# Kernel tuning notes

Measured on AMD Instinct MI355X. Metric: run time of the kernel, lower is better.

## Reference

```python
import jax, jax.numpy as jnp
import numpy as np

T = 16          # timesteps
BATCH = 8       # video clips -> leading dim of x is BATCH*T = 128
C_IN = 768      # fixed by nn.Conv2d(768, redu_dim, 1)
D = 256         # redu_dim
K = 64          # num_centers
H = W = 28
EPS = 1e-12     # torch F.normalize eps


def _conv(x, w, padding):
    # x: [N,C,H,W], w: [O,I,kh,kw]
    return jax.lax.conv_general_dilated(
        x, w, window_strides=(1, 1), padding=padding,
        dimension_numbers=('NCHW', 'OIHW', 'NCHW'))


def setup_inputs() -> dict:
    key = jax.random.key(0)
    ks = jax.random.split(key, 9)
    x = jax.random.normal(ks[0], (BATCH * T, C_IN, H, W), dtype=jnp.float32)
    redu_w = jax.random.normal(ks[1], (D, C_IN, 1, 1), jnp.float32) * 0.02
    redu_b = jnp.zeros((D,), jnp.float32)
    share_w = jax.random.normal(ks[2], (K, D, 1, 1), jnp.float32) * 0.05
    share_b = jnp.zeros((K,), jnp.float32)
    U_z = jax.random.normal(ks[3], (K, K, 3, 3), jnp.float32) * 0.04
    U_r = jax.random.normal(ks[4], (K, K, 3, 3), jnp.float32) * 0.04
    U_h = jax.random.normal(ks[5], (K, K, 3, 3), jnp.float32) * 0.04
    centers = jax.random.normal(ks[6], (K, D), jnp.float32) * 0.06
    return {"x": x, "redu_w": redu_w, "redu_b": redu_b,
            "share_w": share_w, "share_b": share_b,
            "U_z": U_z, "U_r": U_r, "U_h": U_h,
            "centers": centers, "timesteps": T}


def reference(x, redu_w, redu_b, share_w, share_b, U_z, U_r, U_h, centers, timesteps):
    t = timesteps
    bt, _, h, w = x.shape
    b = bt // t
    k = share_w.shape[0]
    d = redu_w.shape[0]

    # channel reduction (1x1 conv)
    xr = _conv(x, redu_w, 'VALID') + redu_b[None, :, None, None]        # [bt,d,h,w]
    # shared assignment logits (1x1 conv)
    wxb = _conv(xr, share_w, 'VALID') + share_b[None, :, None, None]     # [bt,k,h,w]
    wxb = wxb.reshape(b, t, k, h, w).transpose(1, 0, 2, 3, 4)            # [t,b,k,h,w]

    # sequential ConvGRU over timesteps
    h0 = jnp.zeros((b, k, h, w), x.dtype)
    def step(h_tm1, w_t):
        z = jax.nn.sigmoid(w_t + _conv(h_tm1, U_z, 'SAME'))
        r = jax.nn.sigmoid(w_t + _conv(h_tm1, U_r, 'SAME'))
        hh = jnp.tanh(w_t + _conv(r * h_tm1, U_h, 'SAME'))
        h_new = (1.0 - z) * hh + z * h_tm1
        return h_new, h_new
    _, hs = jax.lax.scan(step, h0, wxb)                                  # [t,b,k,h,w]

    assign = hs.transpose(1, 0, 2, 3, 4).reshape(b * t, k, h * w)        # [bt,k,hw]
    # softmax over centers per spatial location
    assign = jax.nn.softmax(assign, axis=1)

    # VLAD aggregation
    a_sum = assign.sum(axis=-1, keepdims=True)                           # [bt,k,1]
    a = a_sum * centers[None]                                            # [bt,k,d]
    xf = xr.reshape(b * t, d, h * w)                                     # [bt,d,hw]
    vlad = jnp.einsum('bkp,bdp->bkd', assign, xf) - a                    # [bt,k,d]

    vlad = vlad.reshape(b, t, k, d).sum(axis=1)                          # [b,k,d]
    # intra-norm over feature dim, then global L2 norm
    vlad = vlad / jnp.maximum(jnp.linalg.norm(vlad, axis=2, keepdims=True), EPS)
    vlad = vlad.reshape(b, k * d)
    vlad = vlad / jnp.maximum(jnp.linalg.norm(vlad, axis=1, keepdims=True), EPS)
    return vlad
```

## Files before the change

kernel.cpp:

```cpp
#include <hip/hip_runtime.h>
#include <hip/hip_bf16.h>

#define T_ 16
#define B_ 8
#define CIN 768
#define D_ 256
#define K_ 64
#define HW 784
#define W_ 28

typedef short short8 __attribute__((ext_vector_type(8)));
typedef short short4v __attribute__((ext_vector_type(4)));
typedef float floatx4 __attribute__((ext_vector_type(4)));
typedef unsigned short ushort_t;

__device__ __forceinline__ unsigned short f2bf(float x) {
    union { float f; unsigned u; } v; v.f = x;
    unsigned u = v.u;
    unsigned r = (u + 0x7fffu + ((u >> 16) & 1u)) >> 16;
    return (unsigned short)r;
}
__device__ __forceinline__ float bf2f(unsigned short h) {
    union { unsigned u; float f; } v; v.u = ((unsigned)h) << 16; return v.f;
}

__device__ __forceinline__ float block_reduce_sum_256(float v) {
    for (int off = 32; off > 0; off >>= 1) v += __shfl_down(v, off, 64);
    __shared__ float red[4];
    __shared__ float tot;
    int lane = threadIdx.x & 63, wid = threadIdx.x >> 6;
    if (lane == 0) red[wid] = v;
    __syncthreads();
    if (threadIdx.x == 0) tot = red[0] + red[1] + red[2] + red[3];
    __syncthreads();
    return tot;
}

__global__ __launch_bounds__(256) void cvt_weights(
    const float* __restrict__ rw, const float* __restrict__ sw,
    const float* __restrict__ Uz, const float* __restrict__ Ur,
    const float* __restrict__ Uh,
    ushort_t* __restrict__ whi, ushort_t* __restrict__ wlo,
    ushort_t* __restrict__ shi, ushort_t* __restrict__ slo,
    ushort_t* __restrict__ azh, ushort_t* __restrict__ azl,
    ushort_t* __restrict__ ahh, ushort_t* __restrict__ ahl)
{
    int i = blockIdx.x * 256 + threadIdx.x;
    const int nR = D_ * CIN;
    const int nS = K_ * D_;
    const int nZR = 128 * 576;
    const int nH = 64 * 576;
    if (i < nR) {
        float x = rw[i];
        unsigned short h = f2bf(x);
        whi[i] = h; wlo[i] = f2bf(x - bf2f(h));
    } else if (i < nR + nS) {
        int j = i - nR;
        float x = sw[j];
        unsigned short h = f2bf(x);
        shi[j] = h; slo[j] = f2bf(x - bf2f(h));
    } else if (i < nR + nS + nZR) {
        int j = i - nR - nS;
        int row = j / 576, kk = j - row * 576;
        int tap = kk >> 6, c = kk & 63;
        const float* U = (row < 64) ? Uz : Ur;
        float x = U[(((size_t)(row & 63)) * 64 + c) * 9 + tap];
        unsigned short h = f2bf(x);
        azh[j] = h; azl[j] = f2bf(x - bf2f(h));
    } else if (i < nR + nS + nZR + nH) {
        int j = i - nR - nS - nZR;
        int row = j / 576, kk = j - row * 576;
        int tap = kk >> 6, c = kk & 63;
        float x = Uh[(((size_t)row) * 64 + c) * 9 + tap];
        unsigned short h = f2bf(x);
        ahh[j] = h; ahl[j] = f2bf(x - bf2f(h));
    }
}

template<int MTOT, int BM, int KD, int MINW>
__global__ __launch_bounds__(256, MINW) void mfma_conv1x1(
    const float* __restrict__ X, const ushort_t* __restrict__ Whi,
    const ushort_t* __restrict__ Wlo, const float* __restrict__ bias,
    float* __restrict__ Out)
{
    const int nt = blockIdx.x, mt = blockIdx.y, bt = blockIdx.z;
    const int p0 = nt * 112, m0 = mt * BM;
    const int tid = threadIdx.x, lane = tid & 63, wv = tid >> 6;
    const int li = lane & 15, koff = (lane >> 4) * 8;
    constexpr int MI = BM / 64;
    constexpr int NKS = KD / 32;
    const float* Xb = X + (size_t)bt * KD * HW;
    float* Ob = Out + (size_t)bt * MTOT * HW;

    __shared__ ushort_t lB[2][112 * 40];

    floatx4 acc[MI][7];
#pragma unroll
    for (int a = 0; a < MI; ++a)
#pragma unroll
        for (int b = 0; b < 7; ++b) acc[a][b] = (floatx4){0.f, 0.f, 0.f, 0.f};

    const int mbase = m0 + wv * (MI * 16);

    const int u0j = tid / 112, u0p = tid - u0j * 112;
    const bool u1v = tid < 192;
    const int u1j = (tid + 256) / 112, u1p = (tid + 256) - u1j * 112;

    float b0[16], b1[16];
    short8 ahi[MI], alo[MI];

    auto loadB = [&](int k0, float* bb) {
        const float* xp0 = Xb + (size_t)(k0 + u0j * 8) * HW + p0 + u0p;
#pragma unroll
        for (int c = 0; c < 8; ++c) bb[c] = xp0[(size_t)c * HW];
        if (u1v) {
            const float* xp1 = Xb + (size_t)(k0 + u1j * 8) * HW + p0 + u1p;
#pragma unroll
            for (int c = 0; c < 8; ++c) bb[8 + c] = xp1[(size_t)c * HW];
        }
    };
    auto writeB = [&](const float* bb) {
        short8 vh, vl;
#pragma unroll
        for (int c = 0; c < 8; ++c) {
            unsigned short h = f2bf(bb[c]);
            vh[c] = (short)h; vl[c] = (short)f2bf(bb[c] - bf2f(h));
        }
        *(short8*)&lB[0][u0p * 40 + u0j * 8] = vh;
        *(short8*)&lB[1][u0p * 40 + u0j * 8] = vl;
        if (u1v) {
#pragma unroll
            for (int c = 0; c < 8; ++c) {
                unsigned short h = f2bf(bb[8 + c]);
                vh[c] = (short)h; vl[c] = (short)f2bf(bb[8 + c] - bf2f(h));
            }
            *(short8*)&lB[0][u1p * 40 + u1j * 8] = vh;
            *(short8*)&lB[1][u1p * 40 + u1j * 8] = vl;
        }
    };
    auto loadA = [&](int k0) {
#pragma unroll
        for (int mi = 0; mi < MI; ++mi) {
            int m = mbase + mi * 16 + li;
            ahi[mi] = *(const short8*)(Whi + (size_t)m * KD + k0 + koff);
            alo[mi] = *(const short8*)(Wlo + (size_t)m * KD + k0 + koff);
        }
    };
    auto domfma = [&]() {
#pragma unroll
        for (int ni = 0; ni < 7; ++ni) {
            int n = ni * 16 + li;
            short8 bhi = *(const short8*)&lB[0][n * 40 + koff];
            short8 blo = *(const short8*)&lB[1][n * 40 + koff];
#pragma unroll
            for (int mi = 0; mi < MI; ++mi) {
                acc[mi][ni] = __builtin_amdgcn_mfma_f32_16x16x32_bf16(ahi[mi], bhi, acc[mi][ni], 0, 0, 0);
                acc[mi][ni] = __builtin_amdgcn_mfma_f32_16x16x32_bf16(ahi[mi], blo, acc[mi][ni], 0, 0, 0);
                acc[mi][ni] = __builtin_amdgcn_mfma_f32_16x16x32_bf16(alo[mi], bhi, acc[mi][ni], 0, 0, 0);
            }
        }
    };

    loadB(0, b0);
    for (int ks = 0; ks < NKS; ks += 2) {
        loadA(ks * 32);
        writeB(b0);
        __syncthreads();
        if (ks + 1 < NKS) loadB((ks + 1) * 32, b1);
        domfma();
        __syncthreads();
        loadA((ks + 1) * 32);
        writeB(b1);
        __syncthreads();
        if (ks + 2 < NKS) loadB((ks + 2) * 32, b0);
        domfma();
        __syncthreads();
    }

#pragma unroll
    for (int mi = 0; mi < MI; ++mi) {
        int m0g = mbase + mi * 16 + ((lane >> 4) << 2);
#pragma unroll
        for (int ni = 0; ni < 7; ++ni) {
            int p = p0 + ni * 16 + li;
#pragma unroll
            for (int r = 0; r < 4; ++r)
                Ob[(size_t)(m0g + r) * HW + p] = acc[mi][ni][r] + bias[m0g + r];
        }
    }
}

__global__ __launch_bounds__(512, 2) void gru_step(
    const ushort_t* __restrict__ hRhi, const ushort_t* __restrict__ hRlo,
    ushort_t* __restrict__ hWhi, ushort_t* __restrict__ hWlo,
    const ushort_t* __restrict__ azh, const ushort_t* __restrict__ azl,
    const ushort_t* __restrict__ ahh, const ushort_t* __restrict__ ahl,
    const float* __restrict__ wxb, float* __restrict__ hs_t, int t)
{
    const int y0 = blockIdx.x, b = blockIdx.y;
    const int tid = threadIdx.x, lane = tid & 63, wv = tid >> 6;
    const int li = lane & 15, koff8 = (lane >> 4) * 8, kq = (lane >> 4) * 4;

    __shared__ ushort_t Hhi[5 * 30 * 72], Hlo[5 * 30 * 72];
    __shared__ ushort_t Rhi[3 * 30 * 72], Rlo[3 * 30 * 72];
    __shared__ float zs[28 * 68];

    {
        const ushort_t* gh = hRhi + (size_t)b * HW * 64;
        const ushort_t* gl = hRlo + (size_t)b * HW * 64;
        for (int e = tid; e < 1200; e += 512) {
            int r = e / 240, rem = e - r * 240;
            int lx = rem >> 3, j = rem & 7;
            int gy = y0 - 2 + r, gx = lx - 1;
            short8 vh = {0,0,0,0,0,0,0,0}, vl = {0,0,0,0,0,0,0,0};
            if (gy >= 0 && gy < 28 && gx >= 0 && gx < 28) {
                size_t go = ((size_t)(gy * 28 + gx)) * 64 + j * 8;
                vh = *(const short8*)(gh + go);
                vl = *(const short8*)(gl + go);
            }
            int lo = (r * 30 + lx) * 72 + j * 8;
            *(short8*)&Hhi[lo] = vh;
            *(short8*)&Hlo[lo] = vl;
        }
        short8 z8 = {0,0,0,0,0,0,0,0};
        for (int e = tid; e < 1620; e += 512) {
            if (e < 810) *(short8*)&Rhi[e * 8] = z8;
            else         *(short8*)&Rlo[(e - 810) * 8] = z8;
        }
    }
    __syncthreads();

    const float* wx = wxb + ((size_t)(b * T_ + t) * K_) * HW;
    const int c0 = li;
    const int c1 = (li < 12) ? 16 + li : 0;

    if (wv < 4) {
        const int kb = wv * 16;
        const ushort_t* Ah = azh + (size_t)(kb + li) * 576;
        const ushort_t* Al = azl + (size_t)(kb + li) * 576;
        floatx4 az[2];
        az[0] = (floatx4){0.f,0.f,0.f,0.f}; az[1] = (floatx4){0.f,0.f,0.f,0.f};
#pragma unroll
        for (int tap = 0; tap < 9; ++tap) {
            const int dy = tap / 3, dx = tap - dy * 3;
#pragma unroll
            for (int ch = 0; ch < 2; ++ch) {
                short8 whi_ = *(const short8*)(Ah + tap * 64 + ch * 32 + koff8);
                short8 wlo_ = *(const short8*)(Al + tap * 64 + ch * 32 + koff8);
                int cb = ch * 32 + koff8;
                int o0 = ((dy + 1) * 30 + c0 + dx) * 72 + cb;
                int o1 = ((dy + 1) * 30 + c1 + dx) * 72 + cb;
                short8 bh0 = *(const short8*)&Hhi[o0];
                short8 bl0 = *(const short8*)&Hlo[o0];
                short8 bh1 = *(const short8*)&Hhi[o1];
                short8 bl1 = *(const short8*)&Hlo[o1];
                az[0] = __builtin_amdgcn_mfma_f32_16x16x32_bf16(whi_, bh0, az[0], 0, 0, 0);
                az[0] = __builtin_amdgcn_mfma_f32_16x16x32_bf16(whi_, bl0, az[0], 0, 0, 0);
                az[0] = __builtin_amdgcn_mfma_f32_16x16x32_bf16(wlo_, bh0, az[0], 0, 0, 0);
                az[1] = __builtin_amdgcn_mfma_f32_16x16x32_bf16(whi_, bh1, az[1], 0, 0, 0);
                az[1] = __builtin_amdgcn_mfma_f32_16x16x32_bf16(whi_, bl1, az[1], 0, 0, 0);
                az[1] = __builtin_amdgcn_mfma_f32_16x16x32_bf16(wlo_, bh1, az[1], 0, 0, 0);
            }
        }
        const int kb4 = kb + kq;
#pragma unroll
        for (int cf = 0; cf < 2; ++cf) {
            int c = cf * 16 + li;
            if (c < 28) {
                floatx4 zv;
#pragma unroll
                for (int r = 0; r < 4; ++r)
                    zv[r] = 1.f / (1.f + __expf(-(wx[(size_t)(kb4 + r) * HW + y0 * 28 + c] + az[cf][r])));
                *(floatx4*)&zs[c * 68 + kb4] = zv;
            }
        }
    } else {
        const int kb = (wv - 4) * 16;
        const ushort_t* Ah = azh + (size_t)(64 + kb + li) * 576;
        const ushort_t* Al = azl + (size_t)(64 + kb + li) * 576;
        floatx4 ar[3][2];
#pragma unroll
        for (int i = 0; i < 3; ++i) {
            ar[i][0] = (floatx4){0.f,0.f,0.f,0.f};
            ar[i][1] = (floatx4){0.f,0.f,0.f,0.f};
        }
        __builtin_amdgcn_s_setprio(1);
#pragma unroll
        for (int tap = 0; tap < 9; ++tap) {
            const int dy = tap / 3, dx = tap - dy * 3;
#pragma unroll
            for (int ch = 0; ch < 2; ++ch) {
                short8 whi_ = *(const short8*)(Ah + tap * 64 + ch * 32 + koff8);
                short8 wlo_ = *(const short8*)(Al + tap * 64 + ch * 32 + koff8);
                int cb = ch * 32 + koff8;
#pragma unroll
                for (int rr = 0; rr < 3; ++rr) {
                    int o0 = ((rr + dy) * 30 + c0 + dx) * 72 + cb;
                    int o1 = ((rr + dy) * 30 + c1 + dx) * 72 + cb;
                    short8 bh0 = *(const short8*)&Hhi[o0];
                    short8 bl0 = *(const short8*)&Hlo[o0];
                    short8 bh1 = *(const short8*)&Hhi[o1];
                    short8 bl1 = *(const short8*)&Hlo[o1];
                    ar[rr][0] = __builtin_amdgcn_mfma_f32_16x16x32_bf16(whi_, bh0, ar[rr][0], 0, 0, 0);
                    ar[rr][0] = __builtin_amdgcn_mfma_f32_16x16x32_bf16(whi_, bl0, ar[rr][0], 0, 0, 0);
                    ar[rr][0] = __builtin_amdgcn_mfma_f32_16x16x32_bf16(wlo_, bh0, ar[rr][0], 0, 0, 0);
                    ar[rr][1] = __builtin_amdgcn_mfma_f32_16x16x32_bf16(whi_, bh1, ar[rr][1], 0, 0, 0);
                    ar[rr][1] = __builtin_amdgcn_mfma_f32_16x16x32_bf16(whi_, bl1, ar[rr][1], 0, 0, 0);
                    ar[rr][1] = __builtin_amdgcn_mfma_f32_16x16x32_bf16(wlo_, bh1, ar[rr][1], 0, 0, 0);
                }
            }
        }
        __builtin_amdgcn_s_setprio(0);
        const int kb4 = kb + kq;
#pragma unroll
        for (int rr = 0; rr < 3; ++rr) {
            int gy = y0 - 1 + rr;
            if (gy < 0 || gy >= 28) continue;
#pragma unroll
            for (int cf = 0; cf < 2; ++cf) {
                int c = cf * 16 + li;
                if (c >= 28) continue;
                short4v ph = *(const short4v*)&Hhi[((rr + 1) * 30 + c + 1) * 72 + kb4];
                short4v pl = *(const short4v*)&Hlo[((rr + 1) * 30 + c + 1) * 72 + kb4];
                short4v vh, vl;
#pragma unroll
                for (int r = 0; r < 4; ++r) {
                    float rv = 1.f / (1.f + __expf(-(wx[(size_t)(kb4 + r) * HW + gy * 28 + c] + ar[rr][cf][r])));
                    float hv = bf2f((unsigned short)ph[r]) + bf2f((unsigned short)pl[r]);
                    float rh = rv * hv;
                    unsigned short h = f2bf(rh);
                    vh[r] = (short)h; vl[r] = (short)f2bf(rh - bf2f(h));
                }
                *(short4v*)&Rhi[(rr * 30 + c + 1) * 72 + kb4] = vh;
                *(short4v*)&Rlo[(rr * 30 + c + 1) * 72 + kb4] = vl;
            }
        }
    }
    __syncthreads();

    if (wv < 4) {
        const int kb = wv * 16;
        const ushort_t* Ah = ahh + (size_t)(kb + li) * 576;
        const ushort_t* Al = ahl + (size_t)(kb + li) * 576;
        floatx4 ac[2];
        ac[0] = (floatx4){0.f,0.f,0.f,0.f}; ac[1] = (floatx4){0.f,0.f,0.f,0.f};
#pragma unroll
        for (int tap = 0; tap < 9; ++tap) {
            const int dy = tap / 3, dx = tap - dy * 3;
#pragma unroll
            for (int ch = 0; ch < 2; ++ch) {
                short8 whi_ = *(const short8*)(Ah + tap * 64 + ch * 32 + koff8);
                short8 wlo_ = *(const short8*)(Al + tap * 64 + ch * 32 + koff8);
                int cb = ch * 32 + koff8;
                int o0 = (dy * 30 + c0 + dx) * 72 + cb;
                int o1 = (dy * 30 + c1 + dx) * 72 + cb;
                short8 bh0 = *(const short8*)&Rhi[o0];
                short8 bl0 = *(const short8*)&Rlo[o0];
                short8 bh1 = *(const short8*)&Rhi[o1];
                short8 bl1 = *(const short8*)&Rlo[o1];
                ac[0] = __builtin_amdgcn_mfma_f32_16x16x32_bf16(whi_, bh0, ac[0], 0, 0, 0);
                ac[0] = __builtin_amdgcn_mfma_f32_16x16x32_bf16(whi_, bl0, ac[0], 0, 0, 0);
                ac[0] = __builtin_amdgcn_mfma_f32_16x16x32_bf16(wlo_, bh0, ac[0], 0, 0, 0);
                ac[1] = __builtin_amdgcn_mfma_f32_16x16x32_bf16(whi_, bh1, ac[1], 0, 0, 0);
                ac[1] = __builtin_amdgcn_mfma_f32_16x16x32_bf16(whi_, bl1, ac[1], 0, 0, 0);
                ac[1] = __builtin_amdgcn_mfma_f32_16x16x32_bf16(wlo_, bh1, ac[1], 0, 0, 0);
            }
        }
        const int kb4 = kb + kq;
        float* hsb = hs_t + (size_t)b * K_ * HW;
#pragma unroll
        for (int cf = 0; cf < 2; ++cf) {
            int c = cf * 16 + li;
            if (c >= 28) continue;
            int p = y0 * 28 + c;
            floatx4 zv = *(const floatx4*)&zs[c * 68 + kb4];
            short4v ph = *(const short4v*)&Hhi[(2 * 30 + c + 1) * 72 + kb4];
            short4v pl = *(const short4v*)&Hlo[(2 * 30 + c + 1) * 72 + kb4];
            short4v vh, vl;
#pragma unroll
            for (int r = 0; r < 4; ++r) {
                int k = kb4 + r;
                float xv = wx[(size_t)k * HW + p] + ac[cf][r];
                float e2 = __expf(2.f * xv);
                float th = 1.f - 2.f / (e2 + 1.f);
                float hp = bf2f((unsigned short)ph[r]) + bf2f((unsigned short)pl[r]);
                float hn = (1.f - zv[r]) * th + zv[r] * hp;
                hsb[(size_t)k * HW + p] = hn;
                unsigned short h = f2bf(hn);
                vh[r] = (short)h; vl[r] = (short)f2bf(hn - bf2f(h));
            }
            size_t o = ((size_t)(b * HW) + p) * 64 + kb4;
            *(short4v*)(hWhi + o) = vh;
            *(short4v*)(hWlo + o) = vl;
        }
    }
}

__global__ __launch_bounds__(256) void softmax_k(float* __restrict__ hs)
{
    int q = blockIdx.x;
    int py = blockIdx.y;
    float* base = hs + (size_t)q * K_ * HW;
    for (int p = py * 392 + threadIdx.x; p < (py + 1) * 392 && p < HW; p += 256) {
        float v[64];
        float m = -1e30f;
#pragma unroll
        for (int k = 0; k < 64; ++k) {
            v[k] = base[(size_t)k * HW + p];
            m = fmaxf(m, v[k]);
        }
        float s = 0.f;
#pragma unroll
        for (int k = 0; k < 64; ++k) {
            v[k] = __expf(v[k] - m);
            s += v[k];
        }
        float inv = 1.f / s;
#pragma unroll
        for (int k = 0; k < 64; ++k)
            base[(size_t)k * HW + p] = v[k] * inv;
    }
}

__global__ __launch_bounds__(256) void vlad_k(const float* __restrict__ assign,
    const float* __restrict__ xr, float* __restrict__ vladt,
    float* __restrict__ asum_bt)
{
    int dt = blockIdx.x, t = blockIdx.y, b = blockIdx.z;
    int q = t * B_ + b, bt = b * T_ + t, d0 = dt * 64;
    const float* ab = assign + (size_t)q * K_ * HW;
    const float* xb = xr + (size_t)bt * D_ * HW;
    __shared__ float As[16][68];
    __shared__ float Xs[16][68];
    int tx = threadIdx.x & 15, ty = threadIdx.x >> 4;
    float acc[4][4] = {{0.f}};
    float pacc[4] = {0.f, 0.f, 0.f, 0.f};

    for (int p0 = 0; p0 < HW; p0 += 16) {
#pragma unroll
        for (int it = 0; it < 4; ++it) {
            int e = threadIdx.x + it * 256;
            int row = e >> 4, pp = e & 15;
            float av_ = ab[(size_t)row * HW + p0 + pp];
            As[pp][row] = av_;
            if (dt == 0) pacc[it] += av_;
            Xs[pp][row] = xb[(size_t)(d0 + row) * HW + p0 + pp];
        }
        __syncthreads();
#pragma unroll
        for (int pp = 0; pp < 16; ++pp) {
            float4 a = *(const float4*)&As[pp][ty * 4];
            float4 xv = *(const float4*)&Xs[pp][tx * 4];
            float av[4] = {a.x, a.y, a.z, a.w};
            float xvv[4] = {xv.x, xv.y, xv.z, xv.w};
#pragma unroll
            for (int r = 0; r < 4; ++r)
#pragma unroll
                for (int s = 0; s < 4; ++s)
                    acc[r][s] = fmaf(av[r], xvv[s], acc[r][s]);
        }
        __syncthreads();
    }
#pragma unroll
    for (int r = 0; r < 4; ++r) {
        int k = ty * 4 + r;
        float4 o = {acc[r][0], acc[r][1], acc[r][2], acc[r][3]};
        *(float4*)&vladt[((size_t)bt * K_ + k) * D_ + d0 + tx * 4] = o;
    }
    if (dt == 0) {
#pragma unroll
        for (int it = 0; it < 4; ++it) {
            float s = pacc[it];
#pragma unroll
            for (int off = 1; off < 16; off <<= 1) s += __shfl_xor(s, off, 16);
            if (tx == 0) asum_bt[(size_t)bt * 64 + ty + it * 16] = s;
        }
    }
}

__global__ __launch_bounds__(256) void norm1_k(const float* __restrict__ vladt,
    const float* __restrict__ asum_bt, const float* __restrict__ centers,
    float* __restrict__ out)
{
    int bid = blockIdx.x; int b = bid >> 6, k = bid & 63; int d = threadIdx.x;
    float acc = 0.f;
#pragma unroll
    for (int t = 0; t < T_; ++t)
        acc += vladt[(((size_t)b * T_ + t) * K_ + k) * D_ + d];
    float asum = 0.f;
#pragma unroll
    for (int t = 0; t < T_; ++t)
        asum += asum_bt[(size_t)(b * T_ + t) * 64 + k];
    acc -= asum * centers[(size_t)k * D_ + d];
    float ss = block_reduce_sum_256(acc * acc);
    float n = fmaxf(sqrtf(ss), 1e-12f);
    out[((size_t)b * K_ + k) * D_ + d] = acc / n;
}

__global__ __launch_bounds__(256) void norm2_k(float* __restrict__ out)
{
    int b = blockIdx.x;
    float* v = out + (size_t)b * (K_ * D_);
    float s = 0.f;
    for (int i = threadIdx.x; i < K_ * D_; i += 256) {
        float x = v[i];
        s = fmaf(x, x, s);
    }
    float tot = block_reduce_sum_256(s);
    float n = fmaxf(sqrtf(tot), 1e-12f);
    for (int i = threadIdx.x; i < K_ * D_; i += 256) v[i] = v[i] / n;
}

extern "C" void kernel_launch(void* const* d_in, const int* in_sizes, int n_in,
                              void* d_out, int out_size, void* d_ws, size_t ws_size,
                              hipStream_t stream)
{
    const float* x       = (const float*)d_in[0];
    const float* redu_w  = (const float*)d_in[1];
    const float* redu_b  = (const float*)d_in[2];
    const float* share_w = (const float*)d_in[3];
    const float* share_b = (const float*)d_in[4];
    const float* Uz      = (const float*)d_in[5];
    const float* Ur      = (const float*)d_in[6];
    const float* Uh      = (const float*)d_in[7];
    const float* centers = (const float*)d_in[8];

    float* ws = (float*)d_ws;
    const size_t SZ_XR   = (size_t)128 * D_ * HW;
    const size_t SZ_WXB  = (size_t)128 * K_ * HW;
    const size_t SZ_HS   = (size_t)T_ * B_ * K_ * HW;
    const size_t SZ_PLANE= (size_t)B_ * K_ * HW;

    float* xr     = ws;
    float* wxb    = xr + SZ_XR;
    float* hs     = wxb + SZ_WXB;
    float* asum_bt= hs + SZ_HS;
    float* wsplit = asum_bt + 8192;
    float* area   = wsplit + 323584;

    ushort_t* whi = (ushort_t*)wsplit;
    ushort_t* wlo = whi + 196608;
    ushort_t* shi = wlo + 196608;
    ushort_t* slo = shi + 16384;
    ushort_t* azh = slo + 16384;
    ushort_t* azl = azh + 73728;
    ushort_t* ahh = azl + 73728;
    ushort_t* ahl = ahh + 36864;

    float* vladt = area;
    ushort_t* st = (ushort_t*)area;
    ushort_t* h0hi = st;
    ushort_t* h0lo = st + SZ_PLANE;
    ushort_t* h1hi = st + 2 * SZ_PLANE;
    ushort_t* h1lo = st + 3 * SZ_PLANE;

    hipMemsetAsync(h0hi, 0, 2 * SZ_PLANE * sizeof(ushort_t), stream);

    cvt_weights<<<dim3((D_ * CIN + K_ * D_ + 128 * 576 + 64 * 576 + 255) / 256),
                  256, 0, stream>>>(redu_w, share_w, Uz, Ur, Uh,
                                    whi, wlo, shi, slo, azh, azl, ahh, ahl);

    mfma_conv1x1<256, 256, CIN, 2><<<dim3(7, 1, 128), 256, 0, stream>>>(x, whi, wlo, redu_b, xr);
    mfma_conv1x1<64, 64, D_, 4><<<dim3(7, 1, 128), 256, 0, stream>>>(xr, shi, slo, share_b, wxb);

    for (int t = 0; t < T_; ++t) {
        const ushort_t* rh_ = (t & 1) ? h1hi : h0hi;
        const ushort_t* rl_ = (t & 1) ? h1lo : h0lo;
        ushort_t* wh_ = (t & 1) ? h0hi : h1hi;
        ushort_t* wl_ = (t & 1) ? h0lo : h1lo;
        gru_step<<<dim3(28, 8), 512, 0, stream>>>(rh_, rl_, wh_, wl_,
                                                  azh, azl, ahh, ahl,
                                                  wxb, hs + (size_t)t * SZ_PLANE, t);
    }

    softmax_k<<<dim3(128, 2), 256, 0, stream>>>(hs);

    vlad_k<<<dim3(4, 16, 8), 256, 0, stream>>>(hs, xr, vladt, asum_bt);
    norm1_k<<<512, 256, 0, stream>>>(vladt, asum_bt, centers, (float*)d_out);
    norm2_k<<<8, 256, 0, stream>>>((float*)d_out);
}
```

Baseline: 647.6 us.

## Process two output rows per GRU step block to cut halo recompute

Each gru_step block now computes two spatial rows instead of one, with enlarged shared H/R tiles and doubled accumulators, and the grid shrinks from 28x8 to 14x8. The r-gate halo recompute drops from three rows per output row to two, and weight fragment loads are shared across two rows. In exchange the grid has only 112 blocks on a many-CU GPU, launch bounds drop to one block per CU, and register pressure rises. The conv1x1 B-load index loses its size_t cast, a minor addressing tweak.

```diff
diff --git a/kernel.cpp b/kernel.cpp
--- a/kernel.cpp
+++ b/kernel.cpp
@@ -112,11 +112,11 @@
     auto loadB = [&](int k0, float* bb) {
         const float* xp0 = Xb + (size_t)(k0 + u0j * 8) * HW + p0 + u0p;
 #pragma unroll
-        for (int c = 0; c < 8; ++c) bb[c] = xp0[(size_t)c * HW];
+        for (int c = 0; c < 8; ++c) bb[c] = xp0[c * HW];
         if (u1v) {
             const float* xp1 = Xb + (size_t)(k0 + u1j * 8) * HW + p0 + u1p;
 #pragma unroll
-            for (int c = 0; c < 8; ++c) bb[8 + c] = xp1[(size_t)c * HW];
+            for (int c = 0; c < 8; ++c) bb[8 + c] = xp1[c * HW];
         }
     };
     auto writeB = [&](const float* bb) {
@@ -190,25 +190,25 @@
     }
 }
 
-__global__ __launch_bounds__(512, 2) void gru_step(
+__global__ __launch_bounds__(512, 1) void gru_step(
     const ushort_t* __restrict__ hRhi, const ushort_t* __restrict__ hRlo,
     ushort_t* __restrict__ hWhi, ushort_t* __restrict__ hWlo,
     const ushort_t* __restrict__ azh, const ushort_t* __restrict__ azl,
     const ushort_t* __restrict__ ahh, const ushort_t* __restrict__ ahl,
     const float* __restrict__ wxb, float* __restrict__ hs_t, int t)
 {
-    const int y0 = blockIdx.x, b = blockIdx.y;
+    const int y0 = blockIdx.x * 2, b = blockIdx.y;
     const int tid = threadIdx.x, lane = tid & 63, wv = tid >> 6;
     const int li = lane & 15, koff8 = (lane >> 4) * 8, kq = (lane >> 4) * 4;
 
-    __shared__ ushort_t Hhi[5 * 30 * 72], Hlo[5 * 30 * 72];
-    __shared__ ushort_t Rhi[3 * 30 * 72], Rlo[3 * 30 * 72];
-    __shared__ float zs[28 * 68];
+    __shared__ ushort_t Hhi[6 * 30 * 72], Hlo[6 * 30 * 72];
+    __shared__ ushort_t Rhi[4 * 30 * 72], Rlo[4 * 30 * 72];
+    __shared__ float zs[2][28 * 68];
 
     {
         const ushort_t* gh = hRhi + (size_t)b * HW * 64;
         const ushort_t* gl = hRlo + (size_t)b * HW * 64;
-        for (int e = tid; e < 1200; e += 512) {
+        for (int e = tid; e < 1440; e += 512) {
             int r = e / 240, rem = e - r * 240;
             int lx = rem >> 3, j = rem & 7;
             int gy = y0 - 2 + r, gx = lx - 1;
@@ -223,9 +223,9 @@
             *(short8*)&Hlo[lo] = vl;
         }
         short8 z8 = {0,0,0,0,0,0,0,0};
-        for (int e = tid; e < 1620; e += 512) {
-            if (e < 810) *(short8*)&Rhi[e * 8] = z8;
-            else         *(short8*)&Rlo[(e - 810) * 8] = z8;
+        for (int e = tid; e < 2160; e += 512) {
+            if (e < 1080) *(short8*)&Rhi[e * 8] = z8;
+            else          *(short8*)&Rlo[(e - 1080) * 8] = z8;
         }
     }
     __syncthreads();
@@ -238,8 +238,12 @@
         const int kb = wv * 16;
         const ushort_t* Ah = azh + (size_t)(kb + li) * 576;
         const ushort_t* Al = azl + (size_t)(kb + li) * 576;
-        floatx4 az[2];
-        az[0] = (floatx4){0.f,0.f,0.f,0.f}; az[1] = (floatx4){0.f,0.f,0.f,0.f};
+        floatx4 az[2][2];
+#pragma unroll
+        for (int yy = 0; yy < 2; ++yy) {
+            az[yy][0] = (floatx4){0.f,0.f,0.f,0.f};
+            az[yy][1] = (floatx4){0.f,0.f,0.f,0.f};
+        }
 #pragma unroll
         for (int tap = 0; tap < 9; ++tap) {
             const int dy = tap / 3, dx = tap - dy * 3;
@@ -248,39 +252,45 @@
                 short8 whi_ = *(const short8*)(Ah + tap * 64 + ch * 32 + koff8);
                 short8 wlo_ = *(const short8*)(Al + tap * 64 + ch * 32 + koff8);
                 int cb = ch * 32 + koff8;
-                int o0 = ((dy + 1) * 30 + c0 + dx) * 72 + cb;
-                int o1 = ((dy + 1) * 30 + c1 + dx) * 72 + cb;
-                short8 bh0 = *(const short8*)&Hhi[o0];
-                short8 bl0 = *(const short8*)&Hlo[o0];
-                short8 bh1 = *(const short8*)&Hhi[o1];
-                short8 bl1 = *(const short8*)&Hlo[o1];
-                az[0] = __builtin_amdgcn_mfma_f32_16x16x32_bf16(whi_, bh0, az[0], 0, 0, 0);
-                az[0] = __builtin_amdgcn_mfma_f32_16x16x32_bf16(whi_, bl0, az[0], 0, 0, 0);
-                az[0] = __builtin_amdgcn_mfma_f32_16x16x32_bf16(wlo_, bh0, az[0], 0, 0, 0);
-                az[1] = __builtin_amdgcn_mfma_f32_16x16x32_bf16(whi_, bh1, az[1], 0, 0, 0);
-                az[1] = __builtin_amdgcn_mfma_f32_16x16x32_bf16(whi_, bl1, az[1], 0, 0, 0);
-                az[1] = __builtin_amdgcn_mfma_f32_16x16x32_bf16(wlo_, bh1, az[1], 0, 0, 0);
+#pragma unroll
+                for (int yy = 0; yy < 2; ++yy) {
+                    int o0 = ((yy + 1 + dy) * 30 + c0 + dx) * 72 + cb;
+                    int o1 = ((yy + 1 + dy) * 30 + c1 + dx) * 72 + cb;
+                    short8 bh0 = *(const short8*)&Hhi[o0];
+                    short8 bl0 = *(const short8*)&Hlo[o0];
+                    short8 bh1 = *(const short8*)&Hhi[o1];
+                    short8 bl1 = *(const short8*)&Hlo[o1];
+                    az[yy][0] = __builtin_amdgcn_mfma_f32_16x16x32_bf16(whi_, bh0, az[yy][0], 0, 0, 0);
+                    az[yy][0] = __builtin_amdgcn_mfma_f32_16x16x32_bf16(whi_, bl0, az[yy][0], 0, 0, 0);
+                    az[yy][0] = __builtin_amdgcn_mfma_f32_16x16x32_bf16(wlo_, bh0, az[yy][0], 0, 0, 0);
+                    az[yy][1] = __builtin_amdgcn_mfma_f32_16x16x32_bf16(whi_, bh1, az[yy][1], 0, 0, 0);
+                    az[yy][1] = __builtin_amdgcn_mfma_f32_16x16x32_bf16(whi_, bl1, az[yy][1], 0, 0, 0);
+                    az[yy][1] = __builtin_amdgcn_mfma_f32_16x16x32_bf16(wlo_, bh1, az[yy][1], 0, 0, 0);
+                }
             }
         }
         const int kb4 = kb + kq;
 #pragma unroll
-        for (int cf = 0; cf < 2; ++cf) {
-            int c = cf * 16 + li;
-            if (c < 28) {
-                floatx4 zv;
-#pragma unroll
-                for (int r = 0; r < 4; ++r)
-                    zv[r] = 1.f / (1.f + __expf(-(wx[(size_t)(kb4 + r) * HW + y0 * 28 + c] + az[cf][r])));
-                *(floatx4*)&zs[c * 68 + kb4] = zv;
+        for (int yy = 0; yy < 2; ++yy) {
+#pragma unroll
+            for (int cf = 0; cf < 2; ++cf) {
+                int c = cf * 16 + li;
+                if (c < 28) {
+                    floatx4 zv;
+#pragma unroll
+                    for (int r = 0; r < 4; ++r)
+                        zv[r] = 1.f / (1.f + __expf(-(wx[(size_t)(kb4 + r) * HW + (y0 + yy) * 28 + c] + az[yy][cf][r])));
+                    *(floatx4*)&zs[yy][c * 68 + kb4] = zv;
+                }
             }
         }
     } else {
         const int kb = (wv - 4) * 16;
         const ushort_t* Ah = azh + (size_t)(64 + kb + li) * 576;
         const ushort_t* Al = azl + (size_t)(64 + kb + li) * 576;
-        floatx4 ar[3][2];
-#pragma unroll
-        for (int i = 0; i < 3; ++i) {
+        floatx4 ar[4][2];
+#pragma unroll
+        for (int i = 0; i < 4; ++i) {
             ar[i][0] = (floatx4){0.f,0.f,0.f,0.f};
             ar[i][1] = (floatx4){0.f,0.f,0.f,0.f};
         }
@@ -294,7 +304,7 @@
                 short8 wlo_ = *(const short8*)(Al + tap * 64 + ch * 32 + koff8);
                 int cb = ch * 32 + koff8;
 #pragma unroll
-                for (int rr = 0; rr < 3; ++rr) {
+                for (int rr = 0; rr < 4; ++rr) {
                     int o0 = ((rr + dy) * 30 + c0 + dx) * 72 + cb;
                     int o1 = ((rr + dy) * 30 + c1 + dx) * 72 + cb;
                     short8 bh0 = *(const short8*)&Hhi[o0];
@@ -313,7 +323,7 @@
         __builtin_amdgcn_s_setprio(0);
         const int kb4 = kb + kq;
 #pragma unroll
-        for (int rr = 0; rr < 3; ++rr) {
+        for (int rr = 0; rr < 4; ++rr) {
             int gy = y0 - 1 + rr;
             if (gy < 0 || gy >= 28) continue;
 #pragma unroll
@@ -342,8 +352,12 @@
         const int kb = wv * 16;
         const ushort_t* Ah = ahh + (size_t)(kb + li) * 576;
         const ushort_t* Al = ahl + (size_t)(kb + li) * 576;
-        floatx4 ac[2];
-        ac[0] = (floatx4){0.f,0.f,0.f,0.f}; ac[1] = (floatx4){0.f,0.f,0.f,0.f};
+        floatx4 ac[2][2];
+#pragma unroll
+        for (int yy = 0; yy < 2; ++yy) {
+            ac[yy][0] = (floatx4){0.f,0.f,0.f,0.f};
+            ac[yy][1] = (floatx4){0.f,0.f,0.f,0.f};
+        }
 #pragma unroll
         for (int tap = 0; tap < 9; ++tap) {
             const int dy = tap / 3, dx = tap - dy * 3;
@@ -352,46 +366,52 @@
                 short8 whi_ = *(const short8*)(Ah + tap * 64 + ch * 32 + koff8);
                 short8 wlo_ = *(const short8*)(Al + tap * 64 + ch * 32 + koff8);
                 int cb = ch * 32 + koff8;
-                int o0 = (dy * 30 + c0 + dx) * 72 + cb;
-                int o1 = (dy * 30 + c1 + dx) * 72 + cb;
-                short8 bh0 = *(const short8*)&Rhi[o0];
-                short8 bl0 = *(const short8*)&Rlo[o0];
-                short8 bh1 = *(const short8*)&Rhi[o1];
-                short8 bl1 = *(const short8*)&Rlo[o1];
-                ac[0] = __builtin_amdgcn_mfma_f32_16x16x32_bf16(whi_, bh0, ac[0], 0, 0, 0);
-                ac[0] = __builtin_amdgcn_mfma_f32_16x16x32_bf16(whi_, bl0, ac[0], 0, 0, 0);
-                ac[0] = __builtin_amdgcn_mfma_f32_16x16x32_bf16(wlo_, bh0, ac[0], 0, 0, 0);
-                ac[1] = __builtin_amdgcn_mfma_f32_16x16x32_bf16(whi_, bh1, ac[1], 0, 0, 0);
-                ac[1] = __builtin_amdgcn_mfma_f32_16x16x32_bf16(whi_, bl1, ac[1], 0, 0, 0);
-                ac[1] = __builtin_amdgcn_mfma_f32_16x16x32_bf16(wlo_, bh1, ac[1], 0, 0, 0);
+#pragma unroll
+                for (int yy = 0; yy < 2; ++yy) {
+                    int o0 = ((yy + dy) * 30 + c0 + dx) * 72 + cb;
+                    int o1 = ((yy + dy) * 30 + c1 + dx) * 72 + cb;
+                    short8 bh0 = *(const short8*)&Rhi[o0];
+                    short8 bl0 = *(const short8*)&Rlo[o0];
+                    short8 bh1 = *(const short8*)&Rhi[o1];
+                    short8 bl1 = *(const short8*)&Rlo[o1];
+                    ac[yy][0] = __builtin_amdgcn_mfma_f32_16x16x32_bf16(whi_, bh0, ac[yy][0], 0, 0, 0);
+                    ac[yy][0] = __builtin_amdgcn_mfma_f32_16x16x32_bf16(whi_, bl0, ac[yy][0], 0, 0, 0);
+                    ac[yy][0] = __builtin_amdgcn_mfma_f32_16x16x32_bf16(wlo_, bh0, ac[yy][0], 0, 0, 0);
+                    ac[yy][1] = __builtin_amdgcn_mfma_f32_16x16x32_bf16(whi_, bh1, ac[yy][1], 0, 0, 0);
+                    ac[yy][1] = __builtin_amdgcn_mfma_f32_16x16x32_bf16(whi_, bl1, ac[yy][1], 0, 0, 0);
+                    ac[yy][1] = __builtin_amdgcn_mfma_f32_16x16x32_bf16(wlo_, bh1, ac[yy][1], 0, 0, 0);
+                }
             }
         }
         const int kb4 = kb + kq;
         float* hsb = hs_t + (size_t)b * K_ * HW;
 #pragma unroll
-        for (int cf = 0; cf < 2; ++cf) {
-            int c = cf * 16 + li;
-            if (c >= 28) continue;
-            int p = y0 * 28 + c;
-            floatx4 zv = *(const floatx4*)&zs[c * 68 + kb4];
-            short4v ph = *(const short4v*)&Hhi[(2 * 30 + c + 1) * 72 + kb4];
-            short4v pl = *(const short4v*)&Hlo[(2 * 30 + c + 1) * 72 + kb4];
-            short4v vh, vl;
-#pragma unroll
-            for (int r = 0; r < 4; ++r) {
-                int k = kb4 + r;
-                float xv = wx[(size_t)k * HW + p] + ac[cf][r];
-                float e2 = __expf(2.f * xv);
-                float th = 1.f - 2.f / (e2 + 1.f);
-                float hp = bf2f((unsigned short)ph[r]) + bf2f((unsigned short)pl[r]);
-                float hn = (1.f - zv[r]) * th + zv[r] * hp;
-                hsb[(size_t)k * HW + p] = hn;
-                unsigned short h = f2bf(hn);
-                vh[r] = (short)h; vl[r] = (short)f2bf(hn - bf2f(h));
-            }
-            size_t o = ((size_t)(b * HW) + p) * 64 + kb4;
-            *(short4v*)(hWhi + o) = vh;
-            *(short4v*)(hWlo + o) = vl;
+        for (int yy = 0; yy < 2; ++yy) {
+#pragma unroll
+            for (int cf = 0; cf < 2; ++cf) {
+                int c = cf * 16 + li;
+                if (c >= 28) continue;
+                int p = (y0 + yy) * 28 + c;
+                floatx4 zv = *(const floatx4*)&zs[yy][c * 68 + kb4];
+                short4v ph = *(const short4v*)&Hhi[((yy + 2) * 30 + c + 1) * 72 + kb4];
+                short4v pl = *(const short4v*)&Hlo[((yy + 2) * 30 + c + 1) * 72 + kb4];
+                short4v vh, vl;
+#pragma unroll
+                for (int r = 0; r < 4; ++r) {
+                    int k = kb4 + r;
+                    float xv = wx[(size_t)k * HW + p] + ac[yy][cf][r];
+                    float e2 = __expf(2.f * xv);
+                    float th = 1.f - 2.f / (e2 + 1.f);
+                    float hp = bf2f((unsigned short)ph[r]) + bf2f((unsigned short)pl[r]);
+                    float hn = (1.f - zv[r]) * th + zv[r] * hp;
+                    hsb[(size_t)k * HW + p] = hn;
+                    unsigned short h = f2bf(hn);
+                    vh[r] = (short)h; vl[r] = (short)f2bf(hn - bf2f(h));
+                }
+                size_t o = ((size_t)(b * HW) + p) * 64 + kb4;
+                *(short4v*)(hWhi + o) = vh;
+                *(short4v*)(hWlo + o) = vl;
+            }
         }
     }
 }
@@ -568,7 +588,7 @@
         const ushort_t* rl_ = (t & 1) ? h1lo : h0lo;
         ushort_t* wh_ = (t & 1) ? h0hi : h1hi;
         ushort_t* wl_ = (t & 1) ? h0lo : h1lo;
-        gru_step<<<dim3(28, 8), 512, 0, stream>>>(rh_, rl_, wh_, wl_,
+        gru_step<<<dim3(14, 8), 512, 0, stream>>>(rh_, rl_, wh_, wl_,
                                                   azh, azl, ahh, ahl,
                                                   wxb, hs + (size_t)t * SZ_PLANE, t);
     }
```

Result: slower. 881.5 us (+36.1%).
